# Kernel tuning notes

Hardware: AMD Instinct MI355X
Metric: run time of the kernel (lower is better)

Reference implementation:

```python
import jax, jax.numpy as jnp
import numpy as np

D_MODEL = 2048
NUM_HEADS = 32
NUM_KV_HEADS = 8
HEAD_DIM = D_MODEL // NUM_HEADS  # 64
GROUP = NUM_HEADS // NUM_KV_HEADS  # 4


def setup_inputs() -> dict:
    key = jax.random.key(0)
    ks = jax.random.split(key, 9)
    s = 1.0 / np.sqrt(D_MODEL)
    kv_dim = NUM_KV_HEADS * HEAD_DIM
    return {
        "x": jax.random.normal(ks[0], (2, 2048, D_MODEL), dtype=jnp.float32),
        "Wq": jax.random.normal(ks[1], (D_MODEL, D_MODEL), dtype=jnp.float32) * s,
        "bq": jnp.zeros((D_MODEL,), dtype=jnp.float32),
        "Wk": jax.random.normal(ks[2], (D_MODEL, kv_dim), dtype=jnp.float32) * s,
        "bk": jnp.zeros((kv_dim,), dtype=jnp.float32),
        "Wv": jax.random.normal(ks[3], (D_MODEL, kv_dim), dtype=jnp.float32) * s,
        "bv": jnp.zeros((kv_dim,), dtype=jnp.float32),
        "Wo": jax.random.normal(ks[4], (D_MODEL, D_MODEL), dtype=jnp.float32) * s,
        "bo": jnp.zeros((D_MODEL,), dtype=jnp.float32),
    }


def reference(x, Wq, bq, Wk, bk, Wv, bv, Wo, bo):
    B, S, _ = x.shape
    # projections
    q = (x @ Wq + bq).reshape(B, S, NUM_HEADS, HEAD_DIM).transpose(0, 2, 1, 3)      # [B,H,S,Dh]
    k = (x @ Wk + bk).reshape(B, S, NUM_KV_HEADS, HEAD_DIM).transpose(0, 2, 1, 3)   # [B,Hkv,S,Dh]
    v = (x @ Wv + bv).reshape(B, S, NUM_KV_HEADS, HEAD_DIM).transpose(0, 2, 1, 3)
    # expand KV heads to match query heads (repeat_interleave along head dim)
    k = jnp.repeat(k, GROUP, axis=1)  # [B,H,S,Dh]
    v = jnp.repeat(v, GROUP, axis=1)
    scale = 1.0 / np.sqrt(HEAD_DIM).astype(np.float32)
    scores = jnp.einsum('bhqd,bhkd->bhqk', q, k) * scale  # [B,H,S,S]
    attn = jax.nn.softmax(scores, axis=-1)
    out = jnp.einsum('bhqk,bhkd->bhqd', attn, v)          # [B,H,S,Dh]
    out = out.transpose(0, 2, 1, 3).reshape(B, S, NUM_HEADS * HEAD_DIM)
    return out @ Wo + bo
```

## Files before the change

### kernel.cpp

```cpp
#include <hip/hip_runtime.h>
#include <stdint.h>

typedef unsigned short u16;
typedef unsigned int u32;
typedef short bf16x8 __attribute__((ext_vector_type(8)));
typedef float f32x4 __attribute__((ext_vector_type(4)));
typedef u32 u32x2 __attribute__((ext_vector_type(2)));

#define GLOAD_LDS16(gptr, lptr)                                                \
  __builtin_amdgcn_global_load_lds(                                            \
      (__attribute__((address_space(1))) void*)(gptr),                         \
      (__attribute__((address_space(3))) void*)(lptr), 16, 0, 0)

#if __has_builtin(__builtin_amdgcn_exp2f)
#define EXP2F(x) __builtin_amdgcn_exp2f(x)
#else
#define EXP2F(x) exp2f(x)
#endif

__device__ __forceinline__ u16 f2bf(float f) {
  union { float f; uint32_t u; } v; v.f = f;
  return (u16)((v.u + 0x7fffu + ((v.u >> 16) & 1u)) >> 16);
}
__device__ __forceinline__ float bf2f(u16 h) {
  union { uint32_t u; float f; } v; v.u = ((uint32_t)h) << 16;
  return v.f;
}
__device__ __forceinline__ u32 cvt_pk_bf16(float lo, float hi) {
  u32 r;
  asm("v_cvt_pk_bf16_f32 %0, %1, %2" : "=v"(r) : "v"(lo), "v"(hi));
  return r;
}

__global__ void k_conv_bf16(const float* __restrict__ src, u16* __restrict__ dst, int n8) {
  int i = blockIdx.x * blockDim.x + threadIdx.x;
  if (i >= n8) return;
  const float4* s = (const float4*)src + (size_t)i * 2;
  float4 a = s[0], b = s[1];
  uint4 o;
  o.x = (uint32_t)f2bf(a.x) | ((uint32_t)f2bf(a.y) << 16);
  o.y = (uint32_t)f2bf(a.z) | ((uint32_t)f2bf(a.w) << 16);
  o.z = (uint32_t)f2bf(b.x) | ((uint32_t)f2bf(b.y) << 16);
  o.w = (uint32_t)f2bf(b.z) | ((uint32_t)f2bf(b.w) << 16);
  ((uint4*)dst)[i] = o;
}

__global__ void k_transpose_bf16(const float* __restrict__ src, u16* __restrict__ dst,
                                 int R, int C) {
  __shared__ float tile[32][33];
  int cb = blockIdx.x * 32, rb = blockIdx.y * 32;
  int tx = threadIdx.x, ty = threadIdx.y;
#pragma unroll
  for (int j = 0; j < 4; ++j)
    tile[ty + j * 8][tx] = src[(size_t)(rb + ty + j * 8) * C + cb + tx];
  __syncthreads();
#pragma unroll
  for (int j = 0; j < 4; ++j)
    dst[(size_t)(cb + ty + j * 8) * R + rb + tx] = f2bf(tile[tx][ty + j * 8]);
}

template <bool BF16OUT>
__global__ __launch_bounds__(256) void k_gemm_bt(
    const u16* __restrict__ A, const u16* __restrict__ Bt,
    const float* __restrict__ bias, void* __restrict__ Cptr,
    int M, int N, int K) {
  __shared__ u16 As[128 * 32];
  __shared__ u16 Bs[128 * 32];
  const int t = threadIdx.x;
  const int lane = t & 63;
  const int w = t >> 6, wr = w >> 1, wc = w & 1;
  const int brow = blockIdx.y * 128, bcol = blockIdx.x * 128;
  const int g = lane >> 4, q = lane & 15;

  f32x4 acc[4][4] = {};
  const int srow = t >> 2;
  const int sj = t & 3;
  const int nkt = K >> 5;
  for (int kt = 0; kt < nkt; ++kt) {
    __syncthreads();
#pragma unroll
    for (int i = 0; i < 2; ++i) {
      int row = srow + i * 64;
      int jsrc = sj ^ ((row >> 1) & 3);
      const u16* ga = A + (size_t)(brow + row) * K + kt * 32 + jsrc * 8;
      const u16* gb = Bt + (size_t)(bcol + row) * K + kt * 32 + jsrc * 8;
      GLOAD_LDS16(ga, (char*)As + i * 4096 + t * 16);
      GLOAD_LDS16(gb, (char*)Bs + i * 4096 + t * 16);
    }
    __syncthreads();
    bf16x8 a[4], b[4];
#pragma unroll
    for (int mt = 0; mt < 4; ++mt) {
      int row = wr * 64 + mt * 16 + q;
      int pos = g ^ ((row >> 1) & 3);
      a[mt] = *(const bf16x8*)(As + row * 32 + pos * 8);
    }
#pragma unroll
    for (int nt = 0; nt < 4; ++nt) {
      int row = wc * 64 + nt * 16 + q;
      int pos = g ^ ((row >> 1) & 3);
      b[nt] = *(const bf16x8*)(Bs + row * 32 + pos * 8);
    }
#pragma unroll
    for (int mt = 0; mt < 4; ++mt)
#pragma unroll
      for (int nt = 0; nt < 4; ++nt)
        acc[mt][nt] = __builtin_amdgcn_mfma_f32_16x16x32_bf16(a[mt], b[nt], acc[mt][nt], 0, 0, 0);
  }
#pragma unroll
  for (int nt = 0; nt < 4; ++nt) {
    int col = bcol + wc * 64 + nt * 16 + q;
    float bv_ = bias[col];
#pragma unroll
    for (int mt = 0; mt < 4; ++mt) {
#pragma unroll
      for (int r = 0; r < 4; ++r) {
        int row = brow + wr * 64 + mt * 16 + g * 4 + r;
        float val = acc[mt][nt][r] + bv_;
        if (BF16OUT)
          ((u16*)Cptr)[(size_t)row * N + col] = f2bf(val);
        else
          ((float*)Cptr)[(size_t)row * N + col] = val;
      }
    }
  }
}

#define LOG2E 1.44269504088896340736f
__global__ __launch_bounds__(256) void k_attn(const u16* __restrict__ qkv,
                                              u16* __restrict__ out) {
  const int qt = blockIdx.x, h = blockIdx.y, b = blockIdx.z;
  const int kvh = h >> 2;
  const int t = threadIdx.x, lane = t & 63, w = t >> 6;
  const int g = lane >> 4, q16 = lane & 15;
  const int LDQ = 3072;

  __shared__ u16 Ksh[64 * 64];
  __shared__ u16 Vsh[64 * 64];
  __shared__ u16 Psh[4][16 * 72] __attribute__((aligned(16)));

  bf16x8 qf[2][2];
#pragma unroll
  for (int sub = 0; sub < 2; ++sub) {
    const size_t qrow = (size_t)(b * 2048 + qt * 128 + sub * 64 + w * 16 + q16);
#pragma unroll
    for (int c = 0; c < 2; ++c) {
      bf16x8 tmp = *(const bf16x8*)(qkv + qrow * LDQ + h * 64 + c * 32 + g * 8);
#pragma unroll
      for (int i = 0; i < 8; ++i)
        tmp[i] = (short)f2bf(bf2f((u16)tmp[i]) * 0.125f);
      qf[sub][c] = tmp;
    }
  }

  f32x4 acc[2][4] = {};
  float m_run[2], l_run[2];
  m_run[0] = m_run[1] = -__builtin_inff();
  l_run[0] = l_run[1] = 0.f;

  const int kbase = b * 2048;
  const int koff = 2048 + kvh * 64;
  const int voff = 2560 + kvh * 64;

  for (int kt = 0; kt < 32; ++kt) {
    __syncthreads();
#pragma unroll
    for (int p = 0; p < 2; ++p) {
      int row = (t >> 3) + p * 32;
      int dc8 = (t & 7) ^ (row & 7);
      const u16* gk = qkv + (size_t)(kbase + kt * 64 + row) * LDQ + koff + dc8 * 8;
      GLOAD_LDS16(gk, (char*)Ksh + p * 4096 + t * 16);
    }
#pragma unroll
    for (int p = 0; p < 2; ++p) {
      int kk = t & 63;
      int dc = (t >> 6) + p * 4;
      bf16x8 vv = *(const bf16x8*)(qkv + (size_t)(kbase + kt * 64 + kk) * LDQ + voff + dc * 8);
#pragma unroll
      for (int i = 0; i < 8; ++i) {
        int d = dc * 8 + i;
        Vsh[d * 64 + (((kk >> 3) ^ (d & 7)) << 3) + (kk & 7)] = (u16)vv[i];
      }
    }
    __syncthreads();

    f32x4 sc[2][4] = {};
#pragma unroll
    for (int c = 0; c < 2; ++c) {
#pragma unroll
      for (int nt = 0; nt < 4; ++nt) {
        int row = nt * 16 + q16;
        bf16x8 kf = *(const bf16x8*)(Ksh + row * 64 + (((c * 4 + g) ^ (row & 7)) << 3));
        sc[0][nt] = __builtin_amdgcn_mfma_f32_16x16x32_bf16(kf, qf[0][c], sc[0][nt], 0, 0, 0);
        sc[1][nt] = __builtin_amdgcn_mfma_f32_16x16x32_bf16(kf, qf[1][c], sc[1][nt], 0, 0, 0);
      }
    }

    bf16x8 pf[2][2];
#pragma unroll
    for (int sub = 0; sub < 2; ++sub) {
      float mt_ = sc[sub][0][0];
#pragma unroll
      for (int nt = 0; nt < 4; ++nt)
#pragma unroll
        for (int r = 0; r < 4; ++r)
          mt_ = fmaxf(mt_, sc[sub][nt][r]);
      mt_ = fmaxf(mt_, __shfl_xor(mt_, 16, 64));
      mt_ = fmaxf(mt_, __shfl_xor(mt_, 32, 64));
      if (__any(mt_ > m_run[sub])) {
        float mn = fmaxf(m_run[sub], mt_);
        float alpha = EXP2F((m_run[sub] - mn) * LOG2E);
        m_run[sub] = mn;
        l_run[sub] *= alpha;
#pragma unroll
        for (int r = 0; r < 4; ++r) {
          float ar = __shfl(alpha, g * 4 + r, 64);
#pragma unroll
          for (int dt = 0; dt < 4; ++dt) acc[sub][dt][r] *= ar;
        }
      }
      float mL = m_run[sub] * LOG2E;
      float lt = 0.f;
#pragma unroll
      for (int nt = 0; nt < 4; ++nt)
#pragma unroll
        for (int r = 0; r < 4; ++r) {
          float p_ = EXP2F(fmaf(sc[sub][nt][r], LOG2E, -mL));
          sc[sub][nt][r] = p_;
          lt += p_;
        }
      lt += __shfl_xor(lt, 16, 64);
      lt += __shfl_xor(lt, 32, 64);
      l_run[sub] += lt;
      u16* prow = &Psh[w][q16 * 72];
#pragma unroll
      for (int nt = 0; nt < 4; ++nt) {
        u32x2 pk;
        pk.x = cvt_pk_bf16(sc[sub][nt][0], sc[sub][nt][1]);
        pk.y = cvt_pk_bf16(sc[sub][nt][2], sc[sub][nt][3]);
        *(u32x2*)(prow + nt * 16 + g * 4) = pk;
      }
      pf[sub][0] = *(const bf16x8*)(&Psh[w][q16 * 72 + g * 8]);
      pf[sub][1] = *(const bf16x8*)(&Psh[w][q16 * 72 + 32 + g * 8]);
    }

#pragma unroll
    for (int c = 0; c < 2; ++c) {
      int kc = c * 4 + g;
#pragma unroll
      for (int dt = 0; dt < 4; ++dt) {
        int d = dt * 16 + q16;
        bf16x8 vf = *(const bf16x8*)(Vsh + d * 64 + ((kc ^ (d & 7)) << 3));
#pragma unroll
        for (int sub = 0; sub < 2; ++sub)
          acc[sub][dt] = __builtin_amdgcn_mfma_f32_16x16x32_bf16(pf[sub][c], vf, acc[sub][dt], 0, 0, 0);
      }
    }
  }

#pragma unroll
  for (int sub = 0; sub < 2; ++sub)
#pragma unroll
    for (int r = 0; r < 4; ++r) {
      float linv = 1.0f / __shfl(l_run[sub], g * 4 + r, 64);
      size_t orow = (size_t)(b * 2048 + qt * 128 + sub * 64 + w * 16 + g * 4 + r);
#pragma unroll
      for (int dt = 0; dt < 4; ++dt)
        out[orow * 2048 + h * 64 + dt * 16 + q16] = f2bf(acc[sub][dt][r] * linv);
    }
}

extern "C" void kernel_launch(void* const* d_in, const int* in_sizes, int n_in,
                              void* d_out, int out_size, void* d_ws, size_t ws_size,
                              hipStream_t stream) {
  const float* x  = (const float*)d_in[0];
  const float* Wq = (const float*)d_in[1];
  const float* bq = (const float*)d_in[2];
  const float* Wk = (const float*)d_in[3];
  const float* bk = (const float*)d_in[4];
  const float* Wv = (const float*)d_in[5];
  const float* bv = (const float*)d_in[6];
  const float* Wo = (const float*)d_in[7];
  const float* bo = (const float*)d_in[8];
  float* out = (float*)d_out;

  char* ws = (char*)d_ws;
  u16*   xb    = (u16*)(ws + 0);
  u16*   wqkvT = (u16*)(ws + 16777216);
  u16*   woT   = (u16*)(ws + 29360128);
  float* bqkv  = (float*)(ws + 37748736);
  u16*   cqkv  = (u16*)(ws + 37761024);
  u16*   aout  = (u16*)(ws + 62926848);
  (void)ws_size; (void)in_sizes; (void)n_in; (void)out_size;

  hipMemcpyAsync(bqkv, bq, 2048 * sizeof(float), hipMemcpyDeviceToDevice, stream);
  hipMemcpyAsync(bqkv + 2048, bk, 512 * sizeof(float), hipMemcpyDeviceToDevice, stream);
  hipMemcpyAsync(bqkv + 2560, bv, 512 * sizeof(float), hipMemcpyDeviceToDevice, stream);

  k_conv_bf16<<<4096, 256, 0, stream>>>(x, xb, 1048576);
  dim3 tb(32, 8);
  k_transpose_bf16<<<dim3(64, 64), tb, 0, stream>>>(Wq, wqkvT, 2048, 2048);
  k_transpose_bf16<<<dim3(16, 64), tb, 0, stream>>>(Wk, wqkvT + 2048 * 2048, 2048, 512);
  k_transpose_bf16<<<dim3(16, 64), tb, 0, stream>>>(Wv, wqkvT + 2560 * 2048, 2048, 512);
  k_transpose_bf16<<<dim3(64, 64), tb, 0, stream>>>(Wo, woT, 2048, 2048);

  k_gemm_bt<true><<<dim3(24, 32), 256, 0, stream>>>(xb, wqkvT, bqkv, cqkv, 4096, 3072, 2048);
  k_attn<<<dim3(16, 32, 2), 256, 0, stream>>>(cqkv, aout);
  k_gemm_bt<false><<<dim3(16, 32), 256, 0, stream>>>(aout, woT, bo, out, 4096, 2048, 2048);
}
```

Measured before the change: 407.9 us.

## Pre-transpose V and double-buffer K/V tiles with async LDS loads in attention

Adds a separate kernel that transposes V into a [b,kvh,d,s] buffer, reusing the x bf16 workspace, so the attention kernel can stage V with direct global-to-LDS loads instead of per-element scattered LDS stores. K and V tiles are double-buffered so the next tile's loads are issued while the current tile is computed, with one barrier per iteration instead of two. MFMA sections are wrapped in s_setprio hints. The cost is an extra kernel launch, a V round-trip through memory, and twice the LDS for K/V, which may lower occupancy.

```diff
diff --git a/kernel.cpp b/kernel.cpp
--- a/kernel.cpp
+++ b/kernel.cpp
@@ -57,6 +57,22 @@
 #pragma unroll
   for (int j = 0; j < 4; ++j)
     dst[(size_t)(cb + ty + j * 8) * R + rb + tx] = f2bf(tile[tx][ty + j * 8]);
+}
+
+__global__ void k_transpose_v(const u16* __restrict__ cqkv, u16* __restrict__ vt) {
+  __shared__ u16 tile[32][34];
+  int st = blockIdx.x, dt = blockIdx.y, bk = blockIdx.z;
+  int b = bk >> 3, kvh = bk & 7;
+  int tx = threadIdx.x, ty = threadIdx.y;
+  const u16* src = cqkv + (size_t)(b * 2048 + st * 32) * 3072 + 2560 + kvh * 64 + dt * 32;
+#pragma unroll
+  for (int j = 0; j < 4; ++j)
+    tile[ty + j * 8][tx] = src[(size_t)(ty + j * 8) * 3072 + tx];
+  __syncthreads();
+  u16* dst = vt + ((size_t)(bk * 64 + dt * 32)) * 2048 + st * 32;
+#pragma unroll
+  for (int j = 0; j < 4; ++j)
+    dst[(size_t)(ty + j * 8) * 2048 + tx] = tile[tx][ty + j * 8];
 }
 
 template <bool BF16OUT>
@@ -128,6 +144,7 @@
 
 #define LOG2E 1.44269504088896340736f
 __global__ __launch_bounds__(256) void k_attn(const u16* __restrict__ qkv,
+                                              const u16* __restrict__ vt,
                                               u16* __restrict__ out) {
   const int qt = blockIdx.x, h = blockIdx.y, b = blockIdx.z;
   const int kvh = h >> 2;
@@ -135,8 +152,8 @@
   const int g = lane >> 4, q16 = lane & 15;
   const int LDQ = 3072;
 
-  __shared__ u16 Ksh[64 * 64];
-  __shared__ u16 Vsh[64 * 64];
+  __shared__ u16 Ksh[2][64 * 64];
+  __shared__ u16 Vsh[2][64 * 64];
   __shared__ u16 Psh[4][16 * 72] __attribute__((aligned(16)));
 
   bf16x8 qf[2][2];
@@ -160,41 +177,44 @@
 
   const int kbase = b * 2048;
   const int koff = 2048 + kvh * 64;
-  const int voff = 2560 + kvh * 64;
+  const u16* vtb = vt + (size_t)((b * 8 + kvh) * 64) * 2048;
+  const int srow = t >> 3;
+  const int sj = t & 7;
+
+  auto stage = [&](int bb, int kt_) {
+#pragma unroll
+    for (int p = 0; p < 2; ++p) {
+      int row = srow + p * 32;
+      int cx = sj ^ (row & 7);
+      const u16* gk = qkv + (size_t)(kbase + kt_ * 64 + row) * LDQ + koff + cx * 8;
+      GLOAD_LDS16(gk, (char*)Ksh[bb] + p * 4096 + t * 16);
+      const u16* gv = vtb + (size_t)row * 2048 + kt_ * 64 + cx * 8;
+      GLOAD_LDS16(gv, (char*)Vsh[bb] + p * 4096 + t * 16);
+    }
+  };
+
+  stage(0, 0);
+  __syncthreads();
+  int cur = 0;
 
   for (int kt = 0; kt < 32; ++kt) {
-    __syncthreads();
-#pragma unroll
-    for (int p = 0; p < 2; ++p) {
-      int row = (t >> 3) + p * 32;
-      int dc8 = (t & 7) ^ (row & 7);
-      const u16* gk = qkv + (size_t)(kbase + kt * 64 + row) * LDQ + koff + dc8 * 8;
-      GLOAD_LDS16(gk, (char*)Ksh + p * 4096 + t * 16);
-    }
-#pragma unroll
-    for (int p = 0; p < 2; ++p) {
-      int kk = t & 63;
-      int dc = (t >> 6) + p * 4;
-      bf16x8 vv = *(const bf16x8*)(qkv + (size_t)(kbase + kt * 64 + kk) * LDQ + voff + dc * 8);
-#pragma unroll
-      for (int i = 0; i < 8; ++i) {
-        int d = dc * 8 + i;
-        Vsh[d * 64 + (((kk >> 3) ^ (d & 7)) << 3) + (kk & 7)] = (u16)vv[i];
-      }
-    }
-    __syncthreads();
+    if (kt < 31) stage(cur ^ 1, kt + 1);
+    const u16* Kc = Ksh[cur];
+    const u16* Vc = Vsh[cur];
 
     f32x4 sc[2][4] = {};
+    __builtin_amdgcn_s_setprio(1);
 #pragma unroll
     for (int c = 0; c < 2; ++c) {
 #pragma unroll
       for (int nt = 0; nt < 4; ++nt) {
         int row = nt * 16 + q16;
-        bf16x8 kf = *(const bf16x8*)(Ksh + row * 64 + (((c * 4 + g) ^ (row & 7)) << 3));
+        bf16x8 kf = *(const bf16x8*)(Kc + row * 64 + (((c * 4 + g) ^ (row & 7)) << 3));
         sc[0][nt] = __builtin_amdgcn_mfma_f32_16x16x32_bf16(kf, qf[0][c], sc[0][nt], 0, 0, 0);
         sc[1][nt] = __builtin_amdgcn_mfma_f32_16x16x32_bf16(kf, qf[1][c], sc[1][nt], 0, 0, 0);
       }
     }
+    __builtin_amdgcn_s_setprio(0);
 
     bf16x8 pf[2][2];
 #pragma unroll
@@ -244,18 +264,22 @@
       pf[sub][1] = *(const bf16x8*)(&Psh[w][q16 * 72 + 32 + g * 8]);
     }
 
+    __builtin_amdgcn_s_setprio(1);
 #pragma unroll
     for (int c = 0; c < 2; ++c) {
       int kc = c * 4 + g;
 #pragma unroll
       for (int dt = 0; dt < 4; ++dt) {
         int d = dt * 16 + q16;
-        bf16x8 vf = *(const bf16x8*)(Vsh + d * 64 + ((kc ^ (d & 7)) << 3));
-#pragma unroll
-        for (int sub = 0; sub < 2; ++sub)
-          acc[sub][dt] = __builtin_amdgcn_mfma_f32_16x16x32_bf16(pf[sub][c], vf, acc[sub][dt], 0, 0, 0);
-      }
-    }
+        bf16x8 vf = *(const bf16x8*)(Vc + d * 64 + ((kc ^ (d & 7)) << 3));
+        acc[0][dt] = __builtin_amdgcn_mfma_f32_16x16x32_bf16(pf[0][c], vf, acc[0][dt], 0, 0, 0);
+        acc[1][dt] = __builtin_amdgcn_mfma_f32_16x16x32_bf16(pf[1][c], vf, acc[1][dt], 0, 0, 0);
+      }
+    }
+    __builtin_amdgcn_s_setprio(0);
+
+    __syncthreads();
+    cur ^= 1;
   }
 
 #pragma unroll
@@ -291,6 +315,7 @@
   float* bqkv  = (float*)(ws + 37748736);
   u16*   cqkv  = (u16*)(ws + 37761024);
   u16*   aout  = (u16*)(ws + 62926848);
+  u16*   vtb   = xb;
   (void)ws_size; (void)in_sizes; (void)n_in; (void)out_size;
 
   hipMemcpyAsync(bqkv, bq, 2048 * sizeof(float), hipMemcpyDeviceToDevice, stream);
@@ -305,6 +330,7 @@
   k_transpose_bf16<<<dim3(64, 64), tb, 0, stream>>>(Wo, woT, 2048, 2048);
 
   k_gemm_bt<true><<<dim3(24, 32), 256, 0, stream>>>(xb, wqkvT, bqkv, cqkv, 4096, 3072, 2048);
-  k_attn<<<dim3(16, 32, 2), 256, 0, stream>>>(cqkv, aout);
+  k_transpose_v<<<dim3(64, 2, 16), tb, 0, stream>>>(cqkv, vtb);
+  k_attn<<<dim3(16, 32, 2), 256, 0, stream>>>(cqkv, vtb, aout);
   k_gemm_bt<false><<<dim3(16, 32), 256, 0, stream>>>(aout, woT, bo, out, 4096, 2048, 2048);
 }
```

New measurement: 397.9 us. -2.4%, faster.
